# Performance work log

Hardware: AMD Instinct MI355X
Metric: run time of the kernel (lower is better)

The kernel has to match this reference:

```python
import jax, jax.numpy as jnp
import numpy as np

T, N, D, H = 256, 128, 1024, 1024  # rollout len, num envs, input dim, hidden dim


def setup_inputs() -> dict:
    key = jax.random.key(0)
    k_x, k_h, k_m, k_wi, k_wh = jax.random.split(key, 5)
    inv_d = 1.0 / np.sqrt(D)
    inv_h = 1.0 / np.sqrt(H)
    return {
        "x": jax.random.normal(k_x, (T * N, D), dtype=jnp.float32),
        "hidden_states": jax.random.normal(k_h, (N, 1, H), dtype=jnp.float32),
        "masks": jax.random.bernoulli(k_m, 0.95, (T * N,)),  # not_dones
        "W_ih": jax.random.normal(k_wi, (3 * H, D), dtype=jnp.float32) * inv_d,
        "W_hh": jax.random.normal(k_wh, (3 * H, H), dtype=jnp.float32) * inv_h,
        "b_ih": jnp.zeros((3 * H,), dtype=jnp.float32),
        "b_hh": jnp.zeros((3 * H,), dtype=jnp.float32),
    }


def reference(x, hidden_states, masks, W_ih, W_hh, b_ih, b_hh):
    """GRU over a (T*N, D) rollout; hidden state is zeroed wherever masks
    (not_dones) is False, exactly matching RNNStateEncoder.seq_forward.
    The torch packed-sequence machinery is an optimization; the math is a
    plain masked sequential GRU.
    """
    n = hidden_states.shape[0]
    h_dim = hidden_states.shape[2]
    t = x.shape[0] // n
    xT = x.reshape(t, n, -1)                      # (T, N, D)
    mT = masks.reshape(t, n).astype(x.dtype)      # (T, N)
    h0 = hidden_states[:, 0, :]                   # num_layers == 1 -> (N, H)

    # Precompute all input projections in one big GEMM: (T, N, 3H)
    x_proj = jnp.einsum('tnd,gd->tng', xT, W_ih) + b_ih

    def step(h, inp):
        xp, m = inp
        h = h * m[:, None]                        # reset at episode boundaries
        hp = h @ W_hh.T + b_hh                    # (N, 3H)
        xr, xz, xn = jnp.split(xp, 3, axis=-1)    # torch gate order: r, z, n
        hr, hz, hn = jnp.split(hp, 3, axis=-1)
        r = jax.nn.sigmoid(xr + hr)
        z = jax.nn.sigmoid(xz + hz)
        ncand = jnp.tanh(xn + r * hn)
        h_new = (1.0 - z) * ncand + z * h
        return h_new, h_new

    h_last, ys = jax.lax.scan(step, h0, (x_proj, mT))
    out = ys.reshape(t * n, h_dim)                # (T*N, H)
    return out, h_last[:, None, :]                # (N, num_layers=1, H)
```

## Files before the change

### kernel.cpp

```cpp
#include <hip/hip_runtime.h>


#define TSTEPS 256
#define NBATCH 128
#define DDIM   1024
#define HDIM   1024

typedef short  bf16x8 __attribute__((ext_vector_type(8)));
typedef float  f32x4  __attribute__((ext_vector_type(4)));
typedef unsigned long long ull;

#define BAR_CTR_OFF  0
#define BAR_GEN_OFF  4
#define MFLAG_OFF    2048
#define FLAGS_OFF    8192
#define WIH_OFF      32768
#define WHH_OFF      (WIH_OFF + 6291456)
#define HF_OFF       (WHH_OFF + 6291456)
#define HHI_OFF      (HF_OFF + 1048576)
#define HLO_OFF      (HHI_OFF + 524288)
#define HP_OFF       (HLO_OFF + 524288)
#define HPBUF        131072ull
#define WS_NEED      (HP_OFF + 257ull * 524288ull)

#define SCOPE_AGENT __HIP_MEMORY_SCOPE_AGENT

__device__ __forceinline__ unsigned short f2bf(float f) {
    union { float f; unsigned u; } v; v.f = f;
    unsigned r = v.u + 0x7FFFu + ((v.u >> 16) & 1u);
    return (unsigned short)(r >> 16);
}
__device__ __forceinline__ float bf2f(unsigned short h) {
    union { unsigned u; float f; } v; v.u = ((unsigned)h) << 16;
    return v.f;
}

__device__ __forceinline__ float mask_val(const void* m, int fmt, int idx) {
    if (fmt == 0) return ((const unsigned char*)m)[idx] ? 1.f : 0.f;
    if (fmt == 1) return ((const int*)m)[idx] ? 1.f : 0.f;
    return (((const float*)m)[idx] != 0.f) ? 1.f : 0.f;
}

__device__ __forceinline__ void st_dev32(unsigned* p, unsigned v) {
    __hip_atomic_store(p, v, __ATOMIC_RELAXED, SCOPE_AGENT);
}

__global__ void detect_mask(const unsigned char* __restrict__ m8, int* __restrict__ flag) {
    __shared__ int s_ones, s_c01, s_cf;
    if (threadIdx.x == 0) { s_ones = 0; s_c01 = 0; s_cf = 0; }
    __syncthreads();
    int ones = 0;
    for (int i = threadIdx.x; i < 4096; i += 256) ones += (m8[i] == 1);
    int c01 = 0, cf = 0;
    const unsigned* m32 = (const unsigned*)m8;
    for (int i = threadIdx.x; i < 1024; i += 256) {
        unsigned v = m32[i];
        c01 += (v <= 1u);
        cf  += (v == 0u || v == 0x3F800000u);
    }
    atomicAdd(&s_ones, ones); atomicAdd(&s_c01, c01); atomicAdd(&s_cf, cf);
    __syncthreads();
    if (threadIdx.x == 0) *flag = (s_ones > 2048) ? 0 : ((s_c01 >= s_cf) ? 1 : 2);
}

__global__ void conv_w(const float* __restrict__ wih, const float* __restrict__ whh,
                       unsigned short* __restrict__ wih_b, unsigned short* __restrict__ whh_b) {
    size_t i = ((size_t)blockIdx.x * 256 + threadIdx.x) * 4;
    if (i >= (size_t)3145728) return;
    float4 a = *(const float4*)(wih + i);
    ushort4 ra; ra.x = f2bf(a.x); ra.y = f2bf(a.y); ra.z = f2bf(a.z); ra.w = f2bf(a.w);
    *(ushort4*)(wih_b + i) = ra;
    float4 b = *(const float4*)(whh + i);
    ushort4 rb; rb.x = f2bf(b.x); rb.y = f2bf(b.y); rb.z = f2bf(b.z); rb.w = f2bf(b.w);
    *(ushort4*)(whh_b + i) = rb;
}

__global__ void init_h(const float* __restrict__ h0, const unsigned char* __restrict__ masks,
                       const int* __restrict__ flag,
                       float* __restrict__ hf, unsigned short* __restrict__ hhi,
                       unsigned short* __restrict__ hlo, unsigned* __restrict__ hp) {
    int i = (blockIdx.x * 256 + threadIdx.x) * 4;
    if (i >= NBATCH * HDIM) return;
    int fmt = *flag;
    int n = i >> 10;
    float m = mask_val(masks, fmt, n);
    float4 a = *(const float4*)(h0 + i);
    float v[4] = { a.x * m, a.y * m, a.z * m, a.w * m };
#pragma unroll
    for (int q = 0; q < 4; ++q) {
        hf[i + q] = v[q];
        unsigned short hi = f2bf(v[q]);
        unsigned short lo = f2bf(v[q] - bf2f(hi));
        hhi[i + q] = hi;
        hlo[i + q] = lo;
        hp[i + q] = ((unsigned)hi << 16) | (unsigned)lo;
    }
}

__launch_bounds__(512, 2)
__global__ void gru_seq(const float* __restrict__ x,
                        const unsigned char* __restrict__ masks,
                        const int* __restrict__ mflag,
                        const float* __restrict__ bih,
                        const float* __restrict__ bhh,
                        const unsigned short* __restrict__ wih,
                        const unsigned short* __restrict__ whh,
                        const float* __restrict__ h0,
                        float* __restrict__ out,
                        unsigned* __restrict__ hp,
                        unsigned* __restrict__ flags) {
    const int bid  = blockIdx.x;
    const int cb   = ((bid >> 5) << 3) | (bid & 7);
    const int rb   = (bid >> 3) & 3;
    const int tid  = threadIdx.x;
    const int wave = tid >> 6;
    const int lane = tid & 63;
    const int l15  = lane & 15;
    const int l4   = lane >> 4;
    const int rt   = wave >> 2;
    const int kq   = wave & 3;
    const int mfmt = *mflag;
    const int an   = rb * 32 + rt * 16 + l15;

    __shared__ __align__(16) unsigned short Wl[49152];
    __shared__ __align__(16) f32x4 Pl[3][512];
    float* Plf = (float*)Pl;

#pragma unroll
    for (int it = 0; it < 12; ++it) {
        const int ck = it * 512 + tid;
        const int sr = ck >> 7;
        const int kc = ck & 127;
        const int grow = (sr >> 4) * 1024 + cb * 16 + (sr & 15);
        bf16x8 v = *(const bf16x8*)(whh + (size_t)grow * 1024 + kc * 8);
        const int byte = (sr * 2048 + kc * 16) ^ ((sr & 7) << 4);
        *(bf16x8*)((char*)Wl + byte) = v;
    }

    const int r = tid >> 4, c = tid & 15;
    const int n = rb * 32 + r;
    const int j = cb * 16 + c;
    const int rtp = r >> 4, ip = r & 3;
    const int lanep = ((r >> 2) & 3) * 16 + c;
    const float bir = bih[j], biz = bih[1024 + j], bin = bih[2048 + j];
    const float bhr = bhh[j], bhz = bhh[1024 + j], bhn = bhh[2048 + j];

    float hold = h0[(size_t)n * 1024 + j] * mask_val(masks, mfmt, n);
    float mn   = mask_val(masks, mfmt, NBATCH + n);

    unsigned* myflag = flags + (rb * 64 + cb) * 16;
    unsigned* pollfl = flags + (rb * 64 + lane) * 16;

    const f32x4 zz = {0.f, 0.f, 0.f, 0.f};

    auto xp_compute = [&](int tt, f32x4* axx) {
        axx[0] = zz; axx[1] = zz; axx[2] = zz;
        const float* xrow = x + ((size_t)tt * NBATCH + an) * 1024 + kq * 256 + l4 * 8;
#pragma unroll
        for (int kt = 0; kt < 8; ++kt) {
            float4 u0 = *(const float4*)(xrow + kt * 32);
            float4 u1 = *(const float4*)(xrow + kt * 32 + 4);
            bf16x8 a;
            a[0] = (short)f2bf(u0.x); a[1] = (short)f2bf(u0.y);
            a[2] = (short)f2bf(u0.z); a[3] = (short)f2bf(u0.w);
            a[4] = (short)f2bf(u1.x); a[5] = (short)f2bf(u1.y);
            a[6] = (short)f2bf(u1.z); a[7] = (short)f2bf(u1.w);
#pragma unroll
            for (int ct = 0; ct < 3; ++ct) {
                const bf16x8 bw = *(const bf16x8*)(wih +
                    (size_t)(ct * 1024 + cb * 16 + l15) * 1024 + kq * 256 + kt * 32 + l4 * 8);
                axx[ct] = __builtin_amdgcn_mfma_f32_16x16x32_bf16(a, bw, axx[ct], 0, 0, 0);
            }
        }
    };
    auto redx = [&](int ct) -> float {
        float s = 0.f;
#pragma unroll
        for (int q = 0; q < 4; ++q)
            s += Plf[((ct * 512 + (rtp * 4 + q) * 64 + lanep) << 2) + ip];
        return s;
    };

    f32x4 axx[3];
    xp_compute(0, axx);
#pragma unroll
    for (int ct = 0; ct < 3; ++ct) Pl[ct][wave * 64 + lane] = axx[ct];
    __syncthreads();
    float xr  = redx(0) + bir;
    float xz  = redx(1) + biz;
    float xn_ = redx(2) + bin;
    __syncthreads();

    for (int t = 0; t < TSTEPS; ++t) {
        const unsigned* hp_c = hp + (size_t)t * HPBUF;
        unsigned*       hp_n = hp + (size_t)(t + 1) * HPBUF;

        uint4 qa[8], qb[8];
        {
            const uint4* hq = (const uint4*)(hp_c + (size_t)an * 1024 + kq * 256 + l4 * 8);
#pragma unroll
            for (int kt = 0; kt < 8; ++kt) { qa[kt] = hq[kt * 8]; qb[kt] = hq[kt * 8 + 1]; }
        }

        if (t < TSTEPS - 1) xp_compute(t + 1, axx);

        f32x4 acch[3]; acch[0] = zz; acch[1] = zz; acch[2] = zz;
#pragma unroll
        for (int kt = 0; kt < 8; ++kt) {
            unsigned e[8];
            e[0] = qa[kt].x; e[1] = qa[kt].y; e[2] = qa[kt].z; e[3] = qa[kt].w;
            e[4] = qb[kt].x; e[5] = qb[kt].y; e[6] = qb[kt].z; e[7] = qb[kt].w;
            bf16x8 ah, al;
#pragma unroll
            for (int i = 0; i < 8; ++i) {
                ah[i] = (short)(e[i] >> 16);
                al[i] = (short)(e[i] & 0xFFFFu);
            }
            const int ktg = kq * 8 + kt;
#pragma unroll
            for (int ct = 0; ct < 3; ++ct) {
                const int sr = ct * 16 + l15;
                const int byte = (sr * 2048 + ktg * 64 + l4 * 16) ^ ((sr & 7) << 4);
                const bf16x8 bw = *(const bf16x8*)((char*)Wl + byte);
                acch[ct] = __builtin_amdgcn_mfma_f32_16x16x32_bf16(ah, bw, acch[ct], 0, 0, 0);
                acch[ct] = __builtin_amdgcn_mfma_f32_16x16x32_bf16(al, bw, acch[ct], 0, 0, 0);
            }
        }
#pragma unroll
        for (int ct = 0; ct < 3; ++ct) Pl[ct][wave * 64 + lane] = acch[ct];
        __syncthreads();

        const float hr = redx(0) + bhr;
        const float hz = redx(1) + bhz;
        const float hn = redx(2) + bhn;
        const float rg = 1.f / (1.f + __expf(-(xr + hr)));
        const float zg = 1.f / (1.f + __expf(-(xz + hz)));
        const float nc = tanhf(xn_ + rg * hn);
        const float hnew = (1.f - zg) * nc + zg * hold;
        __builtin_nontemporal_store(hnew, &out[((size_t)t * NBATCH + n) * HDIM + j]);

        if (t == TSTEPS - 1) {
            __builtin_nontemporal_store(hnew,
                &out[(size_t)TSTEPS * NBATCH * HDIM + (size_t)n * HDIM + j]);
        } else {
            const float hm = hnew * mn;
            hold = hm;
            const unsigned short hi = f2bf(hm);
            const unsigned short lo = f2bf(hm - bf2f(hi));
            st_dev32(&hp_n[(size_t)n * 1024 + j], ((unsigned)hi << 16) | (unsigned)lo);

            asm volatile("s_waitcnt vmcnt(0)" ::: "memory");
            __syncthreads();
            if (tid == 0)
                __hip_atomic_store(myflag, (unsigned)(t + 1), __ATOMIC_RELAXED, SCOPE_AGENT);

#pragma unroll
            for (int ct = 0; ct < 3; ++ct) Pl[ct][wave * 64 + lane] = axx[ct];
            __syncthreads();
            xr  = redx(0) + bir;
            xz  = redx(1) + biz;
            xn_ = redx(2) + bin;
            mn  = (t + 2 < TSTEPS) ? mask_val(masks, mfmt, (t + 2) * NBATCH + n) : 0.f;

            if (wave == 0) {
                const unsigned tgt = (unsigned)(t + 1);
                while (true) {
                    unsigned v = __hip_atomic_load(pollfl, __ATOMIC_RELAXED, SCOPE_AGENT);
                    if (__all((int)(v >= tgt))) break;
                    __builtin_amdgcn_s_sleep(1);
                }
            }
            asm volatile("" ::: "memory");
            __syncthreads();
        }
    }
}

__launch_bounds__(256)
__global__ void gru_main(const float* __restrict__ x,
                         const unsigned char* __restrict__ masks,
                         const float* __restrict__ bih, const float* __restrict__ bhh,
                         const unsigned short* __restrict__ wih,
                         const unsigned short* __restrict__ whh,
                         float* __restrict__ out,
                         float* __restrict__ hf,
                         unsigned short* __restrict__ hhi,
                         unsigned short* __restrict__ hlo,
                         int* __restrict__ bar_ctr, int* __restrict__ bar_gen,
                         const int* __restrict__ mflag) {
    const int bid  = blockIdx.x;
    const int xcd  = bid & 7;
    const int slot = bid >> 3;
    const int cb   = xcd * 2 + (slot >> 2);
    const int rb   = slot & 3;
    const int tid  = threadIdx.x;
    const int wid  = tid >> 6;
    const int lane = tid & 63;
    const int l15  = lane & 15;
    const int l4   = lane >> 4;
    const int mfmt = *mflag;

    __shared__ float xp_l[32][196];
    __shared__ float hp_l[32][196];

    int gbase[3];
#pragma unroll
    for (int c = 0; c < 3; ++c) {
        int ct = wid * 3 + c;
        gbase[c] = (ct >> 2) * 1024 + cb * 64 + (ct & 3) * 16;
    }

    for (int t = 0; t < TSTEPS; ++t) {
        const int cur = t & 1, nxt = cur ^ 1;
        f32x4 accx[2][3], acch[2][3];
        const f32x4 zz = {0.f, 0.f, 0.f, 0.f};
#pragma unroll
        for (int rt = 0; rt < 2; ++rt)
#pragma unroll
            for (int c = 0; c < 3; ++c) { accx[rt][c] = zz; acch[rt][c] = zz; }

        const unsigned short* hhi_c = hhi + (size_t)cur * (NBATCH * HDIM);
        const unsigned short* hlo_c = hlo + (size_t)cur * (NBATCH * HDIM);

        for (int kk = 0; kk < DDIM; kk += 32) {
            const int kb = kk + l4 * 8;
            bf16x8 axh[2], axl[2], ahh[2], ahl[2];
#pragma unroll
            for (int rt = 0; rt < 2; ++rt) {
                const int row = rb * 32 + rt * 16 + l15;
                const float* px = x + ((size_t)(t * NBATCH + row)) * DDIM + kb;
                float4 f0 = *(const float4*)px;
                float4 f1 = *(const float4*)(px + 4);
                float v[8] = { f0.x, f0.y, f0.z, f0.w, f1.x, f1.y, f1.z, f1.w };
#pragma unroll
                for (int qq = 0; qq < 8; ++qq) {
                    unsigned short hi = f2bf(v[qq]);
                    axh[rt][qq] = (short)hi;
                    axl[rt][qq] = (short)f2bf(v[qq] - bf2f(hi));
                }
                const size_t hoff = (size_t)row * HDIM + kb;
                ahh[rt] = *(const bf16x8*)(hhi_c + hoff);
                ahl[rt] = *(const bf16x8*)(hlo_c + hoff);
            }
#pragma unroll
            for (int c = 0; c < 3; ++c) {
                const size_t wrow = (size_t)(gbase[c] + l15) * 1024 + kb;
                const bf16x8 bx = *(const bf16x8*)(wih + wrow);
                const bf16x8 bh = *(const bf16x8*)(whh + wrow);
#pragma unroll
                for (int rt = 0; rt < 2; ++rt) {
                    accx[rt][c] = __builtin_amdgcn_mfma_f32_16x16x32_bf16(axh[rt], bx, accx[rt][c], 0, 0, 0);
                    accx[rt][c] = __builtin_amdgcn_mfma_f32_16x16x32_bf16(axl[rt], bx, accx[rt][c], 0, 0, 0);
                    acch[rt][c] = __builtin_amdgcn_mfma_f32_16x16x32_bf16(ahh[rt], bh, acch[rt][c], 0, 0, 0);
                    acch[rt][c] = __builtin_amdgcn_mfma_f32_16x16x32_bf16(ahl[rt], bh, acch[rt][c], 0, 0, 0);
                }
            }
        }

#pragma unroll
        for (int c = 0; c < 3; ++c) {
            const int ct = wid * 3 + c;
#pragma unroll
            for (int rt = 0; rt < 2; ++rt) {
#pragma unroll
                for (int i = 0; i < 4; ++i) {
                    const int row = rt * 16 + l4 * 4 + i;
                    const int col = ct * 16 + l15;
                    xp_l[row][col] = accx[rt][c][i];
                    hp_l[row][col] = acch[rt][c][i];
                }
            }
        }
        __syncthreads();

#pragma unroll
        for (int u = 0; u < 8; ++u) {
            const int o   = u * 256 + tid;
            const int row = o >> 6;
            const int jj  = o & 63;
            const int nIdx = rb * 32 + row;
            const int gj   = cb * 64 + jj;
            const float xr = xp_l[row][jj],       hr = hp_l[row][jj];
            const float xz = xp_l[row][64 + jj],  hz = hp_l[row][64 + jj];
            const float xn = xp_l[row][128 + jj], hn = hp_l[row][128 + jj];
            const float ar = xr + hr + bih[gj] + bhh[gj];
            const float az = xz + hz + bih[1024 + gj] + bhh[1024 + gj];
            const float rg = 1.f / (1.f + __expf(-ar));
            const float zg = 1.f / (1.f + __expf(-az));
            const float nc = tanhf(xn + bih[2048 + gj] + rg * (hn + bhh[2048 + gj]));
            const float hold = hf[(size_t)cur * (NBATCH * HDIM) + (size_t)nIdx * HDIM + gj];
            const float hnew = (1.f - zg) * nc + zg * hold;
            out[((size_t)t * NBATCH + nIdx) * HDIM + gj] = hnew;
            if (t == TSTEPS - 1) {
                out[(size_t)TSTEPS * NBATCH * HDIM + (size_t)nIdx * HDIM + gj] = hnew;
            } else {
                const float m  = mask_val(masks, mfmt, (t + 1) * NBATCH + nIdx);
                const float hm = hnew * m;
                const size_t ho = (size_t)nxt * (NBATCH * HDIM) + (size_t)nIdx * HDIM + gj;
                hf[ho] = hm;
                const unsigned short hi = f2bf(hm);
                hhi[ho] = hi;
                hlo[ho] = f2bf(hm - bf2f(hi));
            }
        }

        if (t != TSTEPS - 1) {
            __syncthreads();
            if (tid == 0) {
                __threadfence();
                int a = __hip_atomic_fetch_add(bar_ctr, 1, __ATOMIC_ACQ_REL, SCOPE_AGENT);
                if (a == (int)gridDim.x - 1) {
                    __hip_atomic_store(bar_ctr, 0, __ATOMIC_RELAXED, SCOPE_AGENT);
                    __hip_atomic_store(bar_gen, t + 1, __ATOMIC_RELEASE, SCOPE_AGENT);
                } else {
                    while (__hip_atomic_load(bar_gen, __ATOMIC_ACQUIRE, SCOPE_AGENT) < t + 1) {
                        __builtin_amdgcn_s_sleep(16);
                    }
                }
            }
            __syncthreads();
        }
    }
}

extern "C" void kernel_launch(void* const* d_in, const int* in_sizes, int n_in,
                              void* d_out, int out_size, void* d_ws, size_t ws_size,
                              hipStream_t stream) {
    const float* x      = (const float*)d_in[0];
    const float* hidden = (const float*)d_in[1];
    const unsigned char* masks = (const unsigned char*)d_in[2];
    const float* wih    = (const float*)d_in[3];
    const float* whh    = (const float*)d_in[4];
    const float* bih    = (const float*)d_in[5];
    const float* bhh    = (const float*)d_in[6];
    float* out = (float*)d_out;
    char*  ws  = (char*)d_ws;

    hipMemsetAsync(ws, 0, 32768, stream);
    detect_mask<<<1, 256, 0, stream>>>(masks, (int*)(ws + MFLAG_OFF));
    conv_w<<<3072, 256, 0, stream>>>(wih, whh,
                                     (unsigned short*)(ws + WIH_OFF),
                                     (unsigned short*)(ws + WHH_OFF));
    init_h<<<128, 256, 0, stream>>>(hidden, masks, (const int*)(ws + MFLAG_OFF),
                                    (float*)(ws + HF_OFF),
                                    (unsigned short*)(ws + HHI_OFF),
                                    (unsigned short*)(ws + HLO_OFF),
                                    (unsigned*)(ws + HP_OFF));

    if (ws_size >= (size_t)WS_NEED) {
        gru_seq<<<256, 512, 0, stream>>>(x, masks,
                                         (const int*)(ws + MFLAG_OFF),
                                         bih, bhh,
                                         (const unsigned short*)(ws + WIH_OFF),
                                         (const unsigned short*)(ws + WHH_OFF),
                                         hidden, out,
                                         (unsigned*)(ws + HP_OFF),
                                         (unsigned*)(ws + FLAGS_OFF));
    } else {
        gru_main<<<64, 256, 0, stream>>>(x, masks, bih, bhh,
                                         (const unsigned short*)(ws + WIH_OFF),
                                         (const unsigned short*)(ws + WHH_OFF),
                                         out,
                                         (float*)(ws + HF_OFF),
                                         (unsigned short*)(ws + HHI_OFF),
                                         (unsigned short*)(ws + HLO_OFF),
                                         (int*)(ws + BAR_CTR_OFF), (int*)(ws + BAR_GEN_OFF),
                                         (const int*)(ws + MFLAG_OFF));
    }
}
```

Baseline: 3.818 ms.

## Remap blocks, swizzle LDS reduction buffer, ring hidden buffers, defer output store

Changes the block-to-tile mapping so neighbouring block IDs cover different row/column groups, which may change how work spreads across XCDs and how well caches are used. Adds an XOR swizzle to the LDS partial-sum buffer to cut bank conflicts during the cross-wave reduction. Turns the per-timestep hidden-state buffers into a 128-entry ring to shrink the workspace footprint. Moves the output store to after the flag publish so the critical store-then-signal path does not wait on the out write. The ring reuse relies on the barrier keeping no block more than one step ahead.

Result: no change. 3.809 ms (-0.3%).

```diff
diff --git a/kernel.cpp b/kernel.cpp
--- a/kernel.cpp
+++ b/kernel.cpp
@@ -5,6 +5,7 @@
 #define NBATCH 128
 #define DDIM   1024
 #define HDIM   1024
+#define HPW    128
 
 typedef short  bf16x8 __attribute__((ext_vector_type(8)));
 typedef float  f32x4  __attribute__((ext_vector_type(4)));
@@ -21,7 +22,7 @@
 #define HLO_OFF      (HHI_OFF + 524288)
 #define HP_OFF       (HLO_OFF + 524288)
 #define HPBUF        131072ull
-#define WS_NEED      (HP_OFF + 257ull * 524288ull)
+#define WS_NEED      (HP_OFF + (ull)HPW * 524288ull)
 
 #define SCOPE_AGENT __HIP_MEMORY_SCOPE_AGENT
 
@@ -110,8 +111,10 @@
                         unsigned* __restrict__ hp,
                         unsigned* __restrict__ flags) {
     const int bid  = blockIdx.x;
-    const int cb   = ((bid >> 5) << 3) | (bid & 7);
-    const int rb   = (bid >> 3) & 3;
+    const int x7 = bid & 7;
+    const int s5 = bid >> 3;
+    const int cb = ((x7 >> 1) << 4) | (s5 >> 1);
+    const int rb = ((x7 & 1) << 1) | (s5 & 1);
     const int tid  = threadIdx.x;
     const int wave = tid >> 6;
     const int lane = tid & 63;
@@ -124,7 +127,6 @@
 
     __shared__ __align__(16) unsigned short Wl[49152];
     __shared__ __align__(16) f32x4 Pl[3][512];
-    float* Plf = (float*)Pl;
 
 #pragma unroll
     for (int it = 0; it < 12; ++it) {
@@ -152,6 +154,8 @@
     unsigned* pollfl = flags + (rb * 64 + lane) * 16;
 
     const f32x4 zz = {0.f, 0.f, 0.f, 0.f};
+    const int widx  = wave * 64 + lane;
+    const int wbyte = (widx * 16) ^ ((widx & 3) << 5);
 
     auto xp_compute = [&](int tt, f32x4* axx) {
         axx[0] = zz; axx[1] = zz; axx[2] = zz;
@@ -176,15 +180,19 @@
     auto redx = [&](int ct) -> float {
         float s = 0.f;
 #pragma unroll
-        for (int q = 0; q < 4; ++q)
-            s += Plf[((ct * 512 + (rtp * 4 + q) * 64 + lanep) << 2) + ip];
+        for (int q = 0; q < 4; ++q) {
+            const int idx  = (rtp * 4 + q) * 64 + lanep;
+            const int byte = ((idx * 16) ^ ((idx & 3) << 5)) + ip * 4;
+            s += *(const float*)((const char*)Pl + ct * 8192 + byte);
+        }
         return s;
     };
 
     f32x4 axx[3];
     xp_compute(0, axx);
 #pragma unroll
-    for (int ct = 0; ct < 3; ++ct) Pl[ct][wave * 64 + lane] = axx[ct];
+    for (int ct = 0; ct < 3; ++ct)
+        *(f32x4*)((char*)Pl + ct * 8192 + wbyte) = axx[ct];
     __syncthreads();
     float xr  = redx(0) + bir;
     float xz  = redx(1) + biz;
@@ -192,8 +200,8 @@
     __syncthreads();
 
     for (int t = 0; t < TSTEPS; ++t) {
-        const unsigned* hp_c = hp + (size_t)t * HPBUF;
-        unsigned*       hp_n = hp + (size_t)(t + 1) * HPBUF;
+        const unsigned* hp_c = hp + (size_t)(t & (HPW - 1)) * HPBUF;
+        unsigned*       hp_n = hp + (size_t)((t + 1) & (HPW - 1)) * HPBUF;
 
         uint4 qa[8], qb[8];
         {
@@ -227,7 +235,8 @@
             }
         }
 #pragma unroll
-        for (int ct = 0; ct < 3; ++ct) Pl[ct][wave * 64 + lane] = acch[ct];
+        for (int ct = 0; ct < 3; ++ct)
+            *(f32x4*)((char*)Pl + ct * 8192 + wbyte) = acch[ct];
         __syncthreads();
 
         const float hr = redx(0) + bhr;
@@ -237,9 +246,9 @@
         const float zg = 1.f / (1.f + __expf(-(xz + hz)));
         const float nc = tanhf(xn_ + rg * hn);
         const float hnew = (1.f - zg) * nc + zg * hold;
-        __builtin_nontemporal_store(hnew, &out[((size_t)t * NBATCH + n) * HDIM + j]);
 
         if (t == TSTEPS - 1) {
+            __builtin_nontemporal_store(hnew, &out[((size_t)t * NBATCH + n) * HDIM + j]);
             __builtin_nontemporal_store(hnew,
                 &out[(size_t)TSTEPS * NBATCH * HDIM + (size_t)n * HDIM + j]);
         } else {
@@ -254,8 +263,10 @@
             if (tid == 0)
                 __hip_atomic_store(myflag, (unsigned)(t + 1), __ATOMIC_RELAXED, SCOPE_AGENT);
 
-#pragma unroll
-            for (int ct = 0; ct < 3; ++ct) Pl[ct][wave * 64 + lane] = axx[ct];
+            __builtin_nontemporal_store(hnew, &out[((size_t)t * NBATCH + n) * HDIM + j]);
+#pragma unroll
+            for (int ct = 0; ct < 3; ++ct)
+                *(f32x4*)((char*)Pl + ct * 8192 + wbyte) = axx[ct];
             __syncthreads();
             xr  = redx(0) + bir;
             xz  = redx(1) + biz;
```
